# Kernel tuning notes

Hardware: AMD Instinct MI355X
Metric: run time of the kernel (lower is better)

## Reference

```python
import jax, jax.numpy as jnp
import numpy as np

EMBED_DIM = 1024
N_HEADS = 16
HEAD_DIM = EMBED_DIM // N_HEADS  # 64
ROPE_DIM = 4
N_FREQ = HEAD_DIM // (2 * ROPE_DIM)  # 8 rotary freqs per coordinate axis
ROPE_THETA = 10000.0
FFN_DIM = 4 * EMBED_DIM
N_TOK = 4096
N_SEQ = 8
EPS = 1e-5
NEG_INF = -1e30


def setup_inputs() -> dict:
    key = jax.random.key(0)
    ks = jax.random.split(key, 16)
    s = 0.02
    coords = jax.random.uniform(ks[0], (N_TOK, ROPE_DIM), jnp.float32) * 10.0
    feats = jax.random.normal(ks[1], (N_TOK, EMBED_DIM), jnp.float32)
    interior = jnp.sort(jax.random.randint(ks[2], (N_SEQ - 1,), 1, N_TOK)).astype(jnp.int32)
    cu_seqlens = jnp.concatenate([jnp.zeros((1,), jnp.int32), interior,
                                  jnp.full((1,), N_TOK, jnp.int32)])
    # learnable RoPE inverse frequencies, one bank per coordinate axis
    base = 1.0 / (ROPE_THETA ** (jnp.arange(N_FREQ, dtype=jnp.float32) * 2.0 * ROPE_DIM / HEAD_DIM))
    inv_freq = jnp.tile(base[None, :], (ROPE_DIM, 1))  # [rope_dim, n_freq]
    return {
        "coords": coords,
        "feats": feats,
        "cu_seqlens": cu_seqlens,
        "Wqkv": jax.random.normal(ks[3], (EMBED_DIM, 3 * EMBED_DIM), jnp.float32) * s,
        "bqkv": jnp.zeros((3 * EMBED_DIM,), jnp.float32),
        "Wo": jax.random.normal(ks[4], (EMBED_DIM, EMBED_DIM), jnp.float32) * s,
        "bo": jnp.zeros((EMBED_DIM,), jnp.float32),
        "inv_freq": inv_freq,
        "ln1_g": jnp.ones((EMBED_DIM,), jnp.float32),
        "ln1_b": jnp.zeros((EMBED_DIM,), jnp.float32),
        "W1": jax.random.normal(ks[5], (EMBED_DIM, FFN_DIM), jnp.float32) * s,
        "b1": jnp.zeros((FFN_DIM,), jnp.float32),
        "W2": jax.random.normal(ks[6], (FFN_DIM, EMBED_DIM), jnp.float32) * s,
        "b2": jnp.zeros((EMBED_DIM,), jnp.float32),
        "ln2_g": jnp.ones((EMBED_DIM,), jnp.float32),
        "ln2_b": jnp.zeros((EMBED_DIM,), jnp.float32),
    }


def _layernorm(x, g, b):
    mu = jnp.mean(x, axis=-1, keepdims=True)
    xc = x - mu
    var = jnp.mean(xc * xc, axis=-1, keepdims=True)
    return xc * jax.lax.rsqrt(var + EPS) * g + b


def _block_forward(coords, feats, cu_seqlens, Wqkv, bqkv, Wo, bo, inv_freq,
                   ln1_g, ln1_b, W1, b1, W2, b2, ln2_g, ln2_b):
    N, D = feats.shape
    qkv = (feats @ Wqkv + bqkv).reshape(N, 3, N_HEADS, HEAD_DIM)
    q, k, v = qkv[:, 0], qkv[:, 1], qkv[:, 2]  # each [N, H, hd]

    # multi-dimensional learnable RoPE: each coord axis rotates its freq bank
    ang = jnp.einsum('nd,df->ndf', coords, inv_freq).reshape(N, 1, HEAD_DIM // 2)
    cos, sin = jnp.cos(ang), jnp.sin(ang)

    def rot(x):
        x1, x2 = jnp.split(x, 2, axis=-1)
        return jnp.concatenate([x1 * cos - x2 * sin, x2 * cos + x1 * sin], axis=-1)

    q, k = rot(q), rot(k)

    # varlen block-diagonal attention mask from cu_seqlens
    seg = jnp.searchsorted(cu_seqlens[1:], jnp.arange(N), side='right')
    mask = seg[:, None] == seg[None, :]  # [N, N]

    scores = jnp.einsum('nhd,mhd->hnm', q, k) / np.sqrt(HEAD_DIM).astype(np.float32)
    scores = jnp.where(mask[None, :, :], scores, NEG_INF)
    attn = jax.nn.softmax(scores, axis=-1)
    o = jnp.einsum('hnm,mhd->nhd', attn, v).reshape(N, D) @ Wo + bo

    h = _layernorm(feats + o, ln1_g, ln1_b)
    f = jax.nn.gelu(h @ W1 + b1) @ W2 + b2
    return _layernorm(h + f, ln2_g, ln2_b)


def reference(coords, feats, cu_seqlens, Wqkv, bqkv, Wo, bo, inv_freq,
              ln1_g, ln1_b, W1, b1, W2, b2, ln2_g, ln2_b):
    return _block_forward(coords, feats, cu_seqlens, Wqkv, bqkv, Wo, bo, inv_freq,
                          ln1_g, ln1_b, W1, b1, W2, b2, ln2_g, ln2_b)
```

## Files before the change

kernel.cpp:

```cpp
#include <hip/hip_runtime.h>

#define NTOK 4096
#define EMB  1024
#define NH   16
#define HD   64
#define FFN  4096

typedef __bf16 bf16x8 __attribute__((ext_vector_type(8)));
typedef float  f32x4  __attribute__((ext_vector_type(4)));

#define ASG __attribute__((address_space(1)))
#define ASL __attribute__((address_space(3)))

__device__ __forceinline__ float b2f(unsigned short u) {
    union { unsigned int i; float f; } v; v.i = ((unsigned int)u) << 16; return v.f;
}
__device__ __forceinline__ unsigned short f2b(float f) {
    return __builtin_bit_cast(unsigned short, (__bf16)f);
}
__device__ __forceinline__ float ldf(const void* p, size_t i, int f32) {
    return f32 ? ((const float*)p)[i] : b2f(((const unsigned short*)p)[i]);
}
__device__ __forceinline__ int probe_f32(const void* p) {
    return ((const unsigned int*)p)[0] == 0x3F800000u ? 1 : 0;
}
__device__ __forceinline__ float gelu_f(float x) {
    float z = 0.7978845608028654f * (x + 0.044715f * x * x * x);
    float t = 1.0f - 2.0f / (__expf(2.0f * z) + 1.0f);
    return 0.5f * x * (1.0f + t);
}
__device__ __forceinline__ void gll16(const void* g, void* l) {
    __builtin_amdgcn_global_load_lds((const ASG void*)g, (ASL void*)l, 16, 0, 0);
}

__global__ __launch_bounds__(256) void convert_kernel(
    const void* __restrict__ feats, const void* __restrict__ bqkv,
    const void* __restrict__ bo, const void* __restrict__ b1,
    const void* __restrict__ b2, const void* __restrict__ g1,
    const void* __restrict__ e1, const void* __restrict__ g2,
    const void* __restrict__ e2, const int* __restrict__ cu,
    unsigned short* __restrict__ feats_bf, unsigned short* __restrict__ smalls,
    int* __restrict__ seg, const void* __restrict__ pr) {
    const int f32 = probe_f32(pr);
    int bid = blockIdx.x, tid = threadIdx.x;
    if (bid < 4096) {
        size_t base = (size_t)bid * 1024 + tid * 4;
        union { unsigned short u[4]; int2 v; } U;
#pragma unroll
        for (int i = 0; i < 4; ++i) U.u[i] = f2b(ldf(feats, base + i, f32));
        *reinterpret_cast<int2*>(&feats_bf[base]) = U.v;
    } else if (bid < 4109) {
        int flat = (bid - 4096) * 1024 + tid * 4;
        const void* src; int off;
        if      (flat < 3072)  { src = bqkv; off = 0; }
        else if (flat < 4096)  { src = bo;   off = 3072; }
        else if (flat < 8192)  { src = b1;   off = 4096; }
        else if (flat < 9216)  { src = b2;   off = 8192; }
        else if (flat < 10240) { src = g1;   off = 9216; }
        else if (flat < 11264) { src = e1;   off = 10240; }
        else if (flat < 12288) { src = g2;   off = 11264; }
        else                   { src = e2;   off = 12288; }
        union { unsigned short u[4]; int2 v; } U;
#pragma unroll
        for (int i = 0; i < 4; ++i) U.u[i] = f2b(ldf(src, flat - off + i, f32));
        *reinterpret_cast<int2*>(&smalls[flat]) = U.v;
    } else {
        int n = (bid - 4109) * 256 + tid;
        int s = 0;
#pragma unroll
        for (int i = 1; i <= 8; ++i) s += (cu[i] <= n) ? 1 : 0;
        seg[n] = s;
    }
}

__global__ __launch_bounds__(256) void transpose_kernel(
    const void* __restrict__ W, unsigned short* __restrict__ O,
    int K, int N, const void* __restrict__ pr) {
    const int f32 = probe_f32(pr);
    int b = blockIdx.x, tid = threadIdx.x;
    int ntiles = N >> 5;
    int nt = b % ntiles, kt = b / ntiles;
    __shared__ unsigned short T[32][33];
    int x = tid & 31, y = tid >> 5;
#pragma unroll
    for (int i = 0; i < 4; ++i) {
        int k = kt * 32 + y + 8 * i, n = nt * 32 + x;
        T[y + 8 * i][x] = f2b(ldf(W, (size_t)k * N + n, f32));
    }
    __syncthreads();
#pragma unroll
    for (int i = 0; i < 4; ++i) {
        int n = nt * 32 + y + 8 * i, k = kt * 32 + x;
        O[(size_t)n * K + k] = T[x][y + 8 * i];
    }
}

template <int ACT, int OUTEXT, int TN, int SPLITV>
__global__ __launch_bounds__(256) void gemm128(
    const unsigned short* __restrict__ A, const unsigned short* __restrict__ Bt,
    const unsigned short* __restrict__ bias, void* __restrict__ C,
    void* __restrict__ C2,
    int M, int N, int K, int lda, int ldb, const void* __restrict__ pr) {
    constexpr int NB = TN / 32;
    __shared__ __align__(16) unsigned short As[128 * 64];
    __shared__ __align__(16) unsigned short Bs[TN * 64];
    const int f32 = OUTEXT ? probe_f32(pr) : 0;
    const int tid = threadIdx.x;
    const int wave = tid >> 6, lane = tid & 63;
    const int wy = wave >> 1, wx = wave & 1;
    const int qm = lane & 15, quad = lane >> 4;
    int bx, by;
    if ((gridDim.y & 7) == 0) {
        int lin = blockIdx.y * gridDim.x + blockIdx.x;
        int ypg = gridDim.y >> 3;
        int xcd = lin & 7, s = lin >> 3;
        int sy = s / gridDim.x;
        by = xcd * ypg + sy;
        bx = s - sy * gridDim.x;
    } else { bx = blockIdx.x; by = blockIdx.y; }
    const int m0 = by * 128, n0 = bx * TN;
    const int r = lane >> 3, gl = lane & 7;

    f32x4 acc[4][NB];
#pragma unroll
    for (int i = 0; i < 4; ++i)
#pragma unroll
        for (int j = 0; j < NB; ++j) acc[i][j] = (f32x4){0.f, 0.f, 0.f, 0.f};

    const unsigned short* Ab = A  + (size_t)m0 * lda;
    const unsigned short* Bb = Bt + (size_t)n0 * ldb;

    for (int k0 = 0; k0 < K; k0 += 64) {
#pragma unroll
        for (int i = 0; i < 4; ++i) {
            int cc = wave * 4 + i;
            gll16(Ab + (size_t)(8 * cc + r) * lda + k0 + ((gl ^ r) << 3), &As[cc * 512]);
        }
#pragma unroll
        for (int i = 0; i < NB; ++i) {
            int cc = wave * NB + i;
            gll16(Bb + (size_t)(8 * cc + r) * ldb + k0 + ((gl ^ r) << 3), &Bs[cc * 512]);
        }
        __syncthreads();
#pragma unroll
        for (int h = 0; h < 2; ++h) {
            bf16x8 af[4], bfr[NB];
#pragma unroll
            for (int i = 0; i < 4; ++i) {
                int phys = (((h * 4 + quad) ^ (qm & 7)) << 3);
                af[i] = *reinterpret_cast<const bf16x8*>(&As[(64 * wy + 16 * i + qm) * 64 + phys]);
            }
#pragma unroll
            for (int j = 0; j < NB; ++j) {
                int phys = (((h * 4 + quad) ^ (qm & 7)) << 3);
                bfr[j] = *reinterpret_cast<const bf16x8*>(&Bs[((TN / 2) * wx + 16 * j + qm) * 64 + phys]);
            }
#pragma unroll
            for (int i = 0; i < 4; ++i)
#pragma unroll
                for (int j = 0; j < NB; ++j)
                    acc[i][j] = __builtin_amdgcn_mfma_f32_16x16x32_bf16(af[i], bfr[j], acc[i][j], 0, 0, 0);
        }
        __syncthreads();
    }
#pragma unroll
    for (int j = 0; j < NB; ++j) {
        int col = n0 + (TN / 2) * wx + 16 * j + qm;
        float bv = b2f(bias[col]);
        if (SPLITV && n0 >= 2048) {
            int d = col - 2048;
#pragma unroll
            for (int i = 0; i < 4; ++i) {
                int rowb = m0 + 64 * wy + 16 * i + quad * 4;
                union { unsigned short u[4]; int2 v; } U;
#pragma unroll
                for (int rr = 0; rr < 4; ++rr) U.u[rr] = f2b(acc[i][j][rr] + bv);
                *reinterpret_cast<int2*>((unsigned short*)C2 + (size_t)d * 4096 + rowb) = U.v;
            }
        } else {
            const int ldc = SPLITV ? 2048 : N;
#pragma unroll
            for (int i = 0; i < 4; ++i) {
                int rowb = m0 + 64 * wy + 16 * i + quad * 4;
#pragma unroll
                for (int rr = 0; rr < 4; ++rr) {
                    size_t idx = (size_t)(rowb + rr) * ldc + col;
                    float v = acc[i][j][rr] + bv;
                    if (ACT == 1) v = gelu_f(v);
                    if (OUTEXT && f32) ((float*)C)[idx] = v;
                    else               ((unsigned short*)C)[idx] = f2b(v);
                }
            }
        }
    }
}

__global__ __launch_bounds__(256) void rope_kernel(
    const void* __restrict__ coords, const void* __restrict__ inv_freq,
    unsigned short* __restrict__ qk, const void* __restrict__ pr) {
    const int f32 = probe_f32(pr);
    int n = blockIdx.x, tid = threadIdx.x;
#pragma unroll
    for (int it = 0; it < 2; ++it) {
        int idx = tid + it * 256;
        int hh = idx >> 5, f = idx & 31;
        float c  = ldf(coords, n * 4 + (f >> 3), f32);
        float iv = ldf(inv_freq, f, f32);
        float sn, cs;
        sincosf(c * iv, &sn, &cs);
#pragma unroll
        for (int w = 0; w < 2; ++w) {
            size_t base = (size_t)n * 2048 + (size_t)w * 1024 + hh * 64;
            float scl = w ? 1.0f : 0.125f;
            float x1 = b2f(qk[base + f]);
            float x2 = b2f(qk[base + 32 + f]);
            qk[base + f]      = f2b((x1 * cs - x2 * sn) * scl);
            qk[base + 32 + f] = f2b((x2 * cs + x1 * sn) * scl);
        }
    }
}

__global__ __launch_bounds__(256) void attn_part(
    const unsigned short* __restrict__ qk, const unsigned short* __restrict__ vt,
    const int* __restrict__ seg, const int* __restrict__ cu,
    unsigned short* __restrict__ u0, unsigned short* __restrict__ u1,
    unsigned short* __restrict__ u2, float* __restrict__ ml) {
    const int h  = blockIdx.y;
    const int t3 = blockIdx.x / 3;
    const int piece = blockIdx.x - 3 * t3;
    const int t0 = t3 * 64;
    const int tid  = threadIdx.x;
    const int wave = tid >> 6, lane = tid & 63;
    const int qm = lane & 15, quad = lane >> 4;

    __shared__ __align__(16) unsigned short Ks[64][72];
    __shared__ __align__(16) unsigned short Vs[64][72];
    __shared__ __align__(16) unsigned short Ps[64][76];
    __shared__ int segq[64], segk[64];

    const unsigned short* qrow = qk + (size_t)(t0 + 16 * wave + qm) * 2048 + h * 64;
    bf16x8 af0 = *reinterpret_cast<const bf16x8*>(qrow + quad * 8);
    bf16x8 af1 = *reinterpret_cast<const bf16x8*>(qrow + 32 + quad * 8);

    if (tid < 64) segq[tid] = seg[t0 + tid];
    __syncthreads();

    const int kbegA = cu[segq[0]] & ~63;
    const int kendT = cu[segq[63] + 1];
    const int nchunks = (kendT - kbegA + 63) >> 6;
    const int third = (nchunks + 2) / 3;
    const int kb = kbegA + piece * third * 64;
    const int ke = min(kendT, kbegA + (piece + 1) * third * 64);

    int sqr[4];
#pragma unroll
    for (int r = 0; r < 4; ++r) sqr[r] = segq[16 * wave + quad * 4 + r];
    const int wsmin = segq[16 * wave];
    const int wsmax = segq[16 * wave + 15];

    float m[4], l[4];
    f32x4 o[4];
#pragma unroll
    for (int r = 0; r < 4; ++r) { m[r] = -1e30f; l[r] = 0.0f; }
#pragma unroll
    for (int t = 0; t < 4; ++t) o[t] = (f32x4){0.f, 0.f, 0.f, 0.f};

    const int krow = tid >> 2, kdc = (tid & 3) * 16;
    int4 kA, kB, vA, vB; int sg;
#define LOAD_CHUNK(KC)                                                                   \
    {                                                                                    \
        const unsigned short* kp = qk + (size_t)((KC) + krow) * 2048 + 1024 + h * 64 + kdc; \
        kA = *reinterpret_cast<const int4*>(kp);                                         \
        kB = *reinterpret_cast<const int4*>(kp + 8);                                     \
        const unsigned short* vp = vt + (size_t)(h * 64 + krow) * 4096 + (KC) + kdc;     \
        vA = *reinterpret_cast<const int4*>(vp);                                         \
        vB = *reinterpret_cast<const int4*>(vp + 8);                                     \
        sg = 127;                                                                        \
        if (tid < 64 && (KC) + tid < ke) sg = seg[(KC) + tid];                           \
    }

    if (kb < ke) LOAD_CHUNK(kb);

    for (int kc = kb; kc < ke; kc += 64) {
        __syncthreads();
        *reinterpret_cast<int4*>(&Ks[krow][kdc])     = kA;
        *reinterpret_cast<int4*>(&Ks[krow][kdc + 8]) = kB;
        *reinterpret_cast<int4*>(&Vs[krow][kdc])     = vA;
        *reinterpret_cast<int4*>(&Vs[krow][kdc + 8]) = vB;
        if (tid < 64) segk[tid] = sg;
        __syncthreads();

        if (kc + 64 < ke) LOAD_CHUNK(kc + 64);

        const int skmin = segk[0], skmax = segk[63];
        const bool act = !(skmax < wsmin || skmin > wsmax);

        if (act) {
            f32x4 sc[4];
#pragma unroll
            for (int nb = 0; nb < 4; ++nb) {
                bf16x8 bf0 = *reinterpret_cast<const bf16x8*>(&Ks[16 * nb + qm][quad * 8]);
                bf16x8 bf1 = *reinterpret_cast<const bf16x8*>(&Ks[16 * nb + qm][32 + quad * 8]);
                f32x4 s = (f32x4){0.f, 0.f, 0.f, 0.f};
                s = __builtin_amdgcn_mfma_f32_16x16x32_bf16(af0, bf0, s, 0, 0, 0);
                s = __builtin_amdgcn_mfma_f32_16x16x32_bf16(af1, bf1, s, 0, 0, 0);
                sc[nb] = s;
            }
            if (!((skmin == skmax) & (wsmin == wsmax))) {
#pragma unroll
                for (int nb = 0; nb < 4; ++nb) {
                    int sk = segk[16 * nb + qm];
#pragma unroll
                    for (int r = 0; r < 4; ++r)
                        sc[nb][r] = (sk == sqr[r]) ? sc[nb][r] : -1e30f;
                }
            }
            float alpha[4];
#pragma unroll
            for (int r = 0; r < 4; ++r) {
                float v = fmaxf(fmaxf(sc[0][r], sc[1][r]), fmaxf(sc[2][r], sc[3][r]));
                v = fmaxf(v, __shfl_xor(v, 1, 64));
                v = fmaxf(v, __shfl_xor(v, 2, 64));
                v = fmaxf(v, __shfl_xor(v, 4, 64));
                v = fmaxf(v, __shfl_xor(v, 8, 64));
                float mn = fmaxf(m[r], v);
                alpha[r] = __expf(m[r] - mn);
                m[r] = mn;
            }
            float rs[4] = {0.f, 0.f, 0.f, 0.f};
#pragma unroll
            for (int nb = 0; nb < 4; ++nb)
#pragma unroll
                for (int r = 0; r < 4; ++r) {
                    float p = __expf(sc[nb][r] - m[r]);
                    sc[nb][r] = p;
                    rs[r] += p;
                }
#pragma unroll
            for (int r = 0; r < 4; ++r) {
                float v = rs[r];
                v += __shfl_xor(v, 1, 64);
                v += __shfl_xor(v, 2, 64);
                v += __shfl_xor(v, 4, 64);
                v += __shfl_xor(v, 8, 64);
                l[r] = l[r] * alpha[r] + v;
            }
#pragma unroll
            for (int nb = 0; nb < 4; ++nb)
#pragma unroll
                for (int r = 0; r < 4; ++r)
                    Ps[16 * wave + quad * 4 + r][16 * nb + qm] = f2b(sc[nb][r]);
#pragma unroll
            for (int t = 0; t < 4; ++t)
#pragma unroll
                for (int r = 0; r < 4; ++r) o[t][r] *= alpha[r];

            bf16x8 pa0 = *reinterpret_cast<const bf16x8*>(&Ps[16 * wave + qm][quad * 8]);
            bf16x8 pa1 = *reinterpret_cast<const bf16x8*>(&Ps[16 * wave + qm][32 + quad * 8]);
#pragma unroll
            for (int dt = 0; dt < 4; ++dt) {
                bf16x8 vb0 = *reinterpret_cast<const bf16x8*>(&Vs[16 * dt + qm][quad * 8]);
                bf16x8 vb1 = *reinterpret_cast<const bf16x8*>(&Vs[16 * dt + qm][32 + quad * 8]);
                o[dt] = __builtin_amdgcn_mfma_f32_16x16x32_bf16(pa0, vb0, o[dt], 0, 0, 0);
                o[dt] = __builtin_amdgcn_mfma_f32_16x16x32_bf16(pa1, vb1, o[dt], 0, 0, 0);
            }
        }
    }
#undef LOAD_CHUNK
    unsigned short* dst = (piece == 0) ? u0 : ((piece == 1) ? u1 : u2);
#pragma unroll
    for (int dt = 0; dt < 4; ++dt)
#pragma unroll
        for (int r = 0; r < 4; ++r) {
            int row = t0 + 16 * wave + quad * 4 + r;
            dst[(size_t)row * 1024 + h * 64 + 16 * dt + qm] = f2b(o[dt][r]);
        }
    if (qm == 0) {
        float2* ML = (float2*)ml;
#pragma unroll
        for (int r = 0; r < 4; ++r) {
            int row = t0 + 16 * wave + quad * 4 + r;
            ML[((piece * 16 + h) << 12) + row] = make_float2(m[r], l[r]);
        }
    }
}

__global__ __launch_bounds__(256) void combine_kernel(
    const unsigned short* __restrict__ u1, const unsigned short* __restrict__ u2,
    const float* __restrict__ ml, unsigned short* __restrict__ u0out) {
    int n = blockIdx.x, tid = threadIdx.x;
    int d4 = tid * 4, h = tid >> 4;
    const float2* ML = (const float2*)ml;
    float2 p0 = ML[(h << 12) + n];
    float2 p1 = ML[((16 + h) << 12) + n];
    float2 p2 = ML[((32 + h) << 12) + n];
    float M = fmaxf(p0.x, fmaxf(p1.x, p2.x));
    float a0 = __expf(p0.x - M), a1 = __expf(p1.x - M), a2 = __expf(p2.x - M);
    float rcp = 1.0f / (a0 * p0.y + a1 * p1.y + a2 * p2.y);
    size_t ix = (size_t)n * 1024 + d4;
    union { int2 q; unsigned short u[4]; } A, B, Cq, R;
    A.q  = *reinterpret_cast<const int2*>(u0out + ix);
    B.q  = *reinterpret_cast<const int2*>(u1 + ix);
    Cq.q = *reinterpret_cast<const int2*>(u2 + ix);
#pragma unroll
    for (int i = 0; i < 4; ++i)
        R.u[i] = f2b((a0 * b2f(A.u[i]) + a1 * b2f(B.u[i]) + a2 * b2f(Cq.u[i])) * rcp);
    *reinterpret_cast<int2*>(u0out + ix) = R.q;
}

template <int X2EXT, int OUTEXT>
__global__ __launch_bounds__(256) void ln_kernel(
    const unsigned short* __restrict__ x1, const void* __restrict__ x2,
    const unsigned short* __restrict__ g, const unsigned short* __restrict__ b,
    void* __restrict__ out, const void* __restrict__ pr) {
    const int f32 = probe_f32(pr);
    int n = blockIdx.x, tid = threadIdx.x;
    __shared__ float red[8];
    const int d0 = tid * 4;
    const size_t ix0 = (size_t)n * EMB + d0;
    float v[4];
    {
        union { int2 q; unsigned short u[4]; } A;
        A.q = *reinterpret_cast<const int2*>(&x1[ix0]);
        if (X2EXT && f32) {
            float4 B = *reinterpret_cast<const float4*>((const float*)x2 + ix0);
            v[0] = b2f(A.u[0]) + B.x; v[1] = b2f(A.u[1]) + B.y;
            v[2] = b2f(A.u[2]) + B.z; v[3] = b2f(A.u[3]) + B.w;
        } else {
            union { int2 q; unsigned short u[4]; } B;
            B.q = *reinterpret_cast<const int2*>((const unsigned short*)x2 + ix0);
#pragma unroll
            for (int i = 0; i < 4; ++i) v[i] = b2f(A.u[i]) + b2f(B.u[i]);
        }
    }
    float s = v[0] + v[1] + v[2] + v[3];
#pragma unroll
    for (int off = 1; off < 64; off <<= 1) s += __shfl_xor(s, off, 64);
    if ((tid & 63) == 0) red[tid >> 6] = s;
    __syncthreads();
    float mu = (red[0] + red[1] + red[2] + red[3]) * (1.0f / 1024.0f);
    float sq = 0.0f;
#pragma unroll
    for (int i = 0; i < 4; ++i) { float c = v[i] - mu; sq += c * c; }
#pragma unroll
    for (int off = 1; off < 64; off <<= 1) sq += __shfl_xor(sq, off, 64);
    if ((tid & 63) == 0) red[4 + (tid >> 6)] = sq;
    __syncthreads();
    float var = (red[4] + red[5] + red[6] + red[7]) * (1.0f / 1024.0f);
    float rcp = rsqrtf(var + 1e-5f);
    union { int2 q; unsigned short u[4]; } G, Bb;
    G.q  = *reinterpret_cast<const int2*>(&g[d0]);
    Bb.q = *reinterpret_cast<const int2*>(&b[d0]);
    if (OUTEXT && f32) {
        float4 R;
        R.x = (v[0] - mu) * rcp * b2f(G.u[0]) + b2f(Bb.u[0]);
        R.y = (v[1] - mu) * rcp * b2f(G.u[1]) + b2f(Bb.u[1]);
        R.z = (v[2] - mu) * rcp * b2f(G.u[2]) + b2f(Bb.u[2]);
        R.w = (v[3] - mu) * rcp * b2f(G.u[3]) + b2f(Bb.u[3]);
        *reinterpret_cast<float4*>((float*)out + ix0) = R;
    } else {
        union { int2 q; unsigned short u[4]; } R;
#pragma unroll
        for (int i = 0; i < 4; ++i)
            R.u[i] = f2b((v[i] - mu) * rcp * b2f(G.u[i]) + b2f(Bb.u[i]));
        *reinterpret_cast<int2*>((unsigned short*)out + ix0) = R.q;
    }
}

extern "C" void kernel_launch(void* const* d_in, const int* in_sizes, int n_in,
                              void* d_out, int out_size, void* d_ws, size_t ws_size,
                              hipStream_t stream) {
    const void* coords   = d_in[0];
    const void* feats    = d_in[1];
    const int*  cu       = (const int*)d_in[2];
    const void* Wqkv     = d_in[3];
    const void* bqkv     = d_in[4];
    const void* Wo       = d_in[5];
    const void* bo       = d_in[6];
    const void* inv_freq = d_in[7];
    const void* ln1_g    = d_in[8];
    const void* ln1_b    = d_in[9];
    const void* W1       = d_in[10];
    const void* b1       = d_in[11];
    const void* W2       = d_in[12];
    const void* b2       = d_in[13];
    const void* ln2_g    = d_in[14];
    const void* ln2_b    = d_in[15];
    const void* pr = ln1_g;

    char* ws = (char*)d_ws;
    int* seg = (int*)ws;
    unsigned short* smalls   = (unsigned short*)(ws + 16384);
    unsigned short* bqkv_bf  = smalls;
    unsigned short* bo_bf    = smalls + 3072;
    unsigned short* b1_bf    = smalls + 4096;
    unsigned short* b2_bf    = smalls + 8192;
    unsigned short* g1_bf    = smalls + 9216;
    unsigned short* e1_bf    = smalls + 10240;
    unsigned short* g2_bf    = smalls + 11264;
    unsigned short* e2_bf    = smalls + 12288;
    unsigned short* feats_bf = (unsigned short*)(ws + 65536);
    unsigned short* hbuf     = feats_bf;
    unsigned short* W1_t     = (unsigned short*)(ws + 8454144);
    unsigned short* u1buf    = (unsigned short*)(ws + 16842752);
    unsigned short* Wqkv_t   = (unsigned short*)(ws + 18939904);
    unsigned short* qkbuf    = (unsigned short*)(ws + 25231360);
    unsigned short* vtbuf    = (unsigned short*)(ws + 42008576);
    unsigned short* attn_o   = (unsigned short*)(ws + 50397184);
    unsigned short* Wo_t     = (unsigned short*)(ws + 18939904);
    unsigned short* W2_t     = (unsigned short*)(ws + 16842752);
    unsigned short* proj     = (unsigned short*)(ws + 25231360);
    unsigned short* f1       = (unsigned short*)(ws + 25231360);
    float* mlbuf = (float*)d_out;
    unsigned short* u2buf = (unsigned short*)((char*)d_out + 2097152);

    hipLaunchKernelGGL(convert_kernel, dim3(4125), dim3(256), 0, stream,
                       feats, bqkv, bo, b1, b2, ln1_g, ln1_b, ln2_g, ln2_b, cu,
                       feats_bf, smalls, seg, pr);
    hipLaunchKernelGGL(transpose_kernel, dim3(3072), dim3(256), 0, stream,
                       Wqkv, Wqkv_t, 1024, 3072, pr);
    hipLaunchKernelGGL(transpose_kernel, dim3(4096), dim3(256), 0, stream,
                       W1, W1_t, 1024, 4096, pr);
    hipLaunchKernelGGL((gemm128<0, 0, 128, 1>), dim3(24, 32), dim3(256), 0, stream,
                       feats_bf, Wqkv_t, bqkv_bf, qkbuf, vtbuf, NTOK, 3072, 1024, 1024, 1024, pr);
    hipLaunchKernelGGL(rope_kernel, dim3(NTOK), dim3(256), 0, stream,
                       coords, inv_freq, qkbuf, pr);
    hipLaunchKernelGGL(attn_part, dim3(192, NH), dim3(256), 0, stream,
                       qkbuf, vtbuf, seg, cu, attn_o, u1buf, u2buf, mlbuf);
    hipLaunchKernelGGL(combine_kernel, dim3(NTOK), dim3(256), 0, stream,
                       u1buf, u2buf, mlbuf, attn_o);
    hipLaunchKernelGGL(transpose_kernel, dim3(1024), dim3(256), 0, stream,
                       Wo, Wo_t, 1024, 1024, pr);
    hipLaunchKernelGGL((gemm128<0, 0, 64, 0>), dim3(16, 32), dim3(256), 0, stream,
                       attn_o, Wo_t, bo_bf, proj, nullptr, NTOK, 1024, 1024, 1024, 1024, pr);
    hipLaunchKernelGGL(transpose_kernel, dim3(4096), dim3(256), 0, stream,
                       W2, W2_t, 4096, 1024, pr);
    hipLaunchKernelGGL((ln_kernel<0, 0>), dim3(NTOK), dim3(256), 0, stream,
                       feats_bf, proj, g1_bf, e1_bf, hbuf, pr);
    hipLaunchKernelGGL((gemm128<1, 0, 128, 0>), dim3(32, 32), dim3(256), 0, stream,
                       hbuf, W1_t, b1_bf, f1, nullptr, NTOK, 4096, 1024, 1024, 1024, pr);
    hipLaunchKernelGGL((gemm128<0, 1, 64, 0>), dim3(16, 32), dim3(256), 0, stream,
                       f1, W2_t, b2_bf, d_out, nullptr, NTOK, 1024, 4096, 4096, 4096, pr);
    hipLaunchKernelGGL((ln_kernel<1, 1>), dim3(NTOK), dim3(256), 0, stream,
                       hbuf, d_out, g2_bf, e2_bf, d_out, pr);
}
```

Before: 425.1 us.

## Schedule attention tiles longest-first and double-buffer K/V chunks in LDS

Adds a small scheduling kernel that ranks the 64 query tiles by their key-chunk count and writes a permutation. The attention grid is reordered so the heaviest tiles are dispatched first, which reduces tail imbalance caused by variable-length segments. The attention loop also double-buffers the K/V shared-memory tiles, so the next chunk's global load is issued before compute and its LDS store happens after compute, dropping one barrier per iteration. This costs an extra kernel launch and doubles the K/V shared memory, which may lower occupancy.

```diff
diff --git a/kernel.cpp b/kernel.cpp
--- a/kernel.cpp
+++ b/kernel.cpp
@@ -71,6 +71,25 @@
         for (int i = 1; i <= 8; ++i) s += (cu[i] <= n) ? 1 : 0;
         seg[n] = s;
     }
+}
+
+__global__ __launch_bounds__(64) void sched_kernel(
+    const int* __restrict__ seg, const int* __restrict__ cu,
+    int* __restrict__ perm) {
+    __shared__ int w[64];
+    int t = threadIdx.x;
+    int s0 = seg[t * 64], s1 = seg[t * 64 + 63];
+    int kb = cu[s0] & ~63;
+    int kend = cu[s1 + 1];
+    w[t] = (kend - kb + 63) >> 6;
+    __syncthreads();
+    int wt = w[t], r = 0;
+#pragma unroll
+    for (int j = 0; j < 64; ++j) {
+        int wj = w[j];
+        r += (wj > wt || (wj == wt && j < t)) ? 1 : 0;
+    }
+    perm[r] = t;
 }
 
 __global__ __launch_bounds__(256) void transpose_kernel(
@@ -223,20 +242,21 @@
 __global__ __launch_bounds__(256) void attn_part(
     const unsigned short* __restrict__ qk, const unsigned short* __restrict__ vt,
     const int* __restrict__ seg, const int* __restrict__ cu,
+    const int* __restrict__ perm,
     unsigned short* __restrict__ u0, unsigned short* __restrict__ u1,
     unsigned short* __restrict__ u2, float* __restrict__ ml) {
-    const int h  = blockIdx.y;
-    const int t3 = blockIdx.x / 3;
-    const int piece = blockIdx.x - 3 * t3;
+    const int h = blockIdx.x / 3;
+    const int piece = blockIdx.x - 3 * h;
+    const int t3 = perm[blockIdx.y];
     const int t0 = t3 * 64;
     const int tid  = threadIdx.x;
     const int wave = tid >> 6, lane = tid & 63;
     const int qm = lane & 15, quad = lane >> 4;
 
-    __shared__ __align__(16) unsigned short Ks[64][72];
-    __shared__ __align__(16) unsigned short Vs[64][72];
+    __shared__ __align__(16) unsigned short Ks[2][64][72];
+    __shared__ __align__(16) unsigned short Vs[2][64][72];
     __shared__ __align__(16) unsigned short Ps[64][76];
-    __shared__ int segq[64], segk[64];
+    __shared__ int segq[64], segk[2][64];
 
     const unsigned short* qrow = qk + (size_t)(t0 + 16 * wave + qm) * 2048 + h * 64;
     bf16x8 af0 = *reinterpret_cast<const bf16x8*>(qrow + quad * 8);
@@ -279,28 +299,30 @@
         if (tid < 64 && (KC) + tid < ke) sg = seg[(KC) + tid];                           \
     }
 
-    if (kb < ke) LOAD_CHUNK(kb);
+    int cur = 0;
+    if (kb < ke) {
+        LOAD_CHUNK(kb);
+        *reinterpret_cast<int4*>(&Ks[0][krow][kdc])     = kA;
+        *reinterpret_cast<int4*>(&Ks[0][krow][kdc + 8]) = kB;
+        *reinterpret_cast<int4*>(&Vs[0][krow][kdc])     = vA;
+        *reinterpret_cast<int4*>(&Vs[0][krow][kdc + 8]) = vB;
+        if (tid < 64) segk[0][tid] = sg;
+    }
 
     for (int kc = kb; kc < ke; kc += 64) {
+        const bool have_next = (kc + 64 < ke);
+        if (have_next) LOAD_CHUNK(kc + 64);
         __syncthreads();
-        *reinterpret_cast<int4*>(&Ks[krow][kdc])     = kA;
-        *reinterpret_cast<int4*>(&Ks[krow][kdc + 8]) = kB;
-        *reinterpret_cast<int4*>(&Vs[krow][kdc])     = vA;
-        *reinterpret_cast<int4*>(&Vs[krow][kdc + 8]) = vB;
-        if (tid < 64) segk[tid] = sg;
-        __syncthreads();
-
-        if (kc + 64 < ke) LOAD_CHUNK(kc + 64);
-
-        const int skmin = segk[0], skmax = segk[63];
+
+        const int skmin = segk[cur][0], skmax = segk[cur][63];
         const bool act = !(skmax < wsmin || skmin > wsmax);
 
         if (act) {
             f32x4 sc[4];
 #pragma unroll
             for (int nb = 0; nb < 4; ++nb) {
-                bf16x8 bf0 = *reinterpret_cast<const bf16x8*>(&Ks[16 * nb + qm][quad * 8]);
-                bf16x8 bf1 = *reinterpret_cast<const bf16x8*>(&Ks[16 * nb + qm][32 + quad * 8]);
+                bf16x8 bf0 = *reinterpret_cast<const bf16x8*>(&Ks[cur][16 * nb + qm][quad * 8]);
+                bf16x8 bf1 = *reinterpret_cast<const bf16x8*>(&Ks[cur][16 * nb + qm][32 + quad * 8]);
                 f32x4 s = (f32x4){0.f, 0.f, 0.f, 0.f};
                 s = __builtin_amdgcn_mfma_f32_16x16x32_bf16(af0, bf0, s, 0, 0, 0);
                 s = __builtin_amdgcn_mfma_f32_16x16x32_bf16(af1, bf1, s, 0, 0, 0);
@@ -309,7 +331,7 @@
             if (!((skmin == skmax) & (wsmin == wsmax))) {
 #pragma unroll
                 for (int nb = 0; nb < 4; ++nb) {
-                    int sk = segk[16 * nb + qm];
+                    int sk = segk[cur][16 * nb + qm];
 #pragma unroll
                     for (int r = 0; r < 4; ++r)
                         sc[nb][r] = (sk == sqr[r]) ? sc[nb][r] : -1e30f;
@@ -359,12 +381,20 @@
             bf16x8 pa1 = *reinterpret_cast<const bf16x8*>(&Ps[16 * wave + qm][32 + quad * 8]);
 #pragma unroll
             for (int dt = 0; dt < 4; ++dt) {
-                bf16x8 vb0 = *reinterpret_cast<const bf16x8*>(&Vs[16 * dt + qm][quad * 8]);
-                bf16x8 vb1 = *reinterpret_cast<const bf16x8*>(&Vs[16 * dt + qm][32 + quad * 8]);
+                bf16x8 vb0 = *reinterpret_cast<const bf16x8*>(&Vs[cur][16 * dt + qm][quad * 8]);
+                bf16x8 vb1 = *reinterpret_cast<const bf16x8*>(&Vs[cur][16 * dt + qm][32 + quad * 8]);
                 o[dt] = __builtin_amdgcn_mfma_f32_16x16x32_bf16(pa0, vb0, o[dt], 0, 0, 0);
                 o[dt] = __builtin_amdgcn_mfma_f32_16x16x32_bf16(pa1, vb1, o[dt], 0, 0, 0);
             }
         }
+        if (have_next) {
+            *reinterpret_cast<int4*>(&Ks[cur ^ 1][krow][kdc])     = kA;
+            *reinterpret_cast<int4*>(&Ks[cur ^ 1][krow][kdc + 8]) = kB;
+            *reinterpret_cast<int4*>(&Vs[cur ^ 1][krow][kdc])     = vA;
+            *reinterpret_cast<int4*>(&Vs[cur ^ 1][krow][kdc + 8]) = vB;
+            if (tid < 64) segk[cur ^ 1][tid] = sg;
+        }
+        cur ^= 1;
     }
 #undef LOAD_CHUNK
     unsigned short* dst = (piece == 0) ? u0 : ((piece == 1) ? u1 : u2);
@@ -499,6 +529,7 @@
     unsigned short* e1_bf    = smalls + 10240;
     unsigned short* g2_bf    = smalls + 11264;
     unsigned short* e2_bf    = smalls + 12288;
+    int* perm                = (int*)(ws + 49152);
     unsigned short* feats_bf = (unsigned short*)(ws + 65536);
     unsigned short* hbuf     = feats_bf;
     unsigned short* W1_t     = (unsigned short*)(ws + 8454144);
@@ -517,6 +548,8 @@
     hipLaunchKernelGGL(convert_kernel, dim3(4125), dim3(256), 0, stream,
                        feats, bqkv, bo, b1, b2, ln1_g, ln1_b, ln2_g, ln2_b, cu,
                        feats_bf, smalls, seg, pr);
+    hipLaunchKernelGGL(sched_kernel, dim3(1), dim3(64), 0, stream,
+                       seg, cu, perm);
     hipLaunchKernelGGL(transpose_kernel, dim3(3072), dim3(256), 0, stream,
                        Wqkv, Wqkv_t, 1024, 3072, pr);
     hipLaunchKernelGGL(transpose_kernel, dim3(4096), dim3(256), 0, stream,
@@ -525,8 +558,8 @@
                        feats_bf, Wqkv_t, bqkv_bf, qkbuf, vtbuf, NTOK, 3072, 1024, 1024, 1024, pr);
     hipLaunchKernelGGL(rope_kernel, dim3(NTOK), dim3(256), 0, stream,
                        coords, inv_freq, qkbuf, pr);
-    hipLaunchKernelGGL(attn_part, dim3(192, NH), dim3(256), 0, stream,
-                       qkbuf, vtbuf, seg, cu, attn_o, u1buf, u2buf, mlbuf);
+    hipLaunchKernelGGL(attn_part, dim3(48, 64), dim3(256), 0, stream,
+                       qkbuf, vtbuf, seg, cu, perm, attn_o, u1buf, u2buf, mlbuf);
     hipLaunchKernelGGL(combine_kernel, dim3(NTOK), dim3(256), 0, stream,
                        u1buf, u2buf, mlbuf, attn_o);
     hipLaunchKernelGGL(transpose_kernel, dim3(1024), dim3(256), 0, stream,
```

New measurement: 415.7 us. 2.2% less time.
